# Optimization experiments

Hardware: AMD Instinct MI355X
Metric: run time of the kernel (lower is better)

Reference implementation:

```python
import jax, jax.numpy as jnp
import numpy as np

N_S, N_C, N_L = 100000, 20000, 5000
E_U, E_T = 2000000, 500000
D_S, D_C, D_L, H = 64, 32, 128, 128
N_LAYERS = 3  # num_layers=2 -> ModuleList holds 3 hetero layers


def _sage(h_src, h_dst, src_idx, dst_idx, W_self, W_neigh, b, n_dst):
    # DGL SAGEConv 'mean': fc_self(h_dst) + fc_neigh(mean of in-neighbor src feats) + bias
    summed = jax.ops.segment_sum(h_src[src_idx], dst_idx, num_segments=n_dst)  # [n_dst, d]
    deg = jax.ops.segment_sum(jnp.ones((src_idx.shape[0],), h_src.dtype), dst_idx, num_segments=n_dst)
    h_neigh = summed / jnp.maximum(deg, 1.0)[:, None]
    return h_dst @ W_self + h_neigh @ W_neigh + b


def setup_inputs() -> dict:
    key = jax.random.key(0)
    ks = jax.random.split(key, 24)
    s = 0.05
    inp = {
        'feat_student': jax.random.normal(ks[0], (N_S, D_S), jnp.float32),
        'feat_concept': jax.random.normal(ks[1], (N_C, D_C), jnp.float32),
        'feat_lecture': jax.random.normal(ks[2], (N_L, D_L), jnp.float32),
        'W_fs': jax.random.normal(ks[3], (D_S, H), jnp.float32) * s,
        'b_fs': jnp.zeros((H,), jnp.float32),
        'W_fc': jax.random.normal(ks[4], (D_C, H), jnp.float32) * s,
        'b_fc': jnp.zeros((H,), jnp.float32),
        'W_fl': jax.random.normal(ks[5], (D_L, H), jnp.float32) * s,
        'b_fl': jnp.zeros((H,), jnp.float32),
        # per-layer, per-relation SAGE params (all dims 128 so they stack)
        'W_self_u': jax.random.normal(ks[6], (N_LAYERS, H, H), jnp.float32) * s,
        'W_neigh_u': jax.random.normal(ks[7], (N_LAYERS, H, H), jnp.float32) * s,
        'b_u': jnp.zeros((N_LAYERS, H), jnp.float32),
        'W_self_t': jax.random.normal(ks[8], (N_LAYERS, H, H), jnp.float32) * s,
        'W_neigh_t': jax.random.normal(ks[9], (N_LAYERS, H, H), jnp.float32) * s,
        'b_t': jnp.zeros((N_LAYERS, H), jnp.float32),
        'und_src': jax.random.randint(ks[10], (E_U,), 0, N_S, jnp.int32),
        'und_dst': jax.random.randint(ks[11], (E_U,), 0, N_C, jnp.int32),
        'tea_src': jax.random.randint(ks[12], (E_T,), 0, N_L, jnp.int32),
        'tea_dst': jax.random.randint(ks[13], (E_T,), 0, N_C, jnp.int32),
    }
    return inp


def reference(feat_student, feat_concept, feat_lecture,
              W_fs, b_fs, W_fc, b_fc, W_fl, b_fl,
              W_self_u, W_neigh_u, b_u, W_self_t, W_neigh_t, b_t,
              und_src, und_dst, tea_src, tea_dst):
    # input projections per node type
    h_s = feat_student @ W_fs + b_fs
    h_c = feat_concept @ W_fc + b_fc
    h_l = feat_lecture @ W_fl + b_fl
    n_c = h_c.shape[0]
    for i in range(N_LAYERS):
        ou = _sage(h_s, h_c, und_src, und_dst, W_self_u[i], W_neigh_u[i], b_u[i], n_c)
        ot = _sage(h_l, h_c, tea_src, tea_dst, W_self_t[i], W_neigh_t[i], b_t[i], n_c)
        # HeteroGraphConv cross-relation aggregate: 'mean' on layer 0, default 'sum' after
        h_c = (ou + ot) * (0.5 if i == 0 else 1.0)
        if i != N_LAYERS - 1:
            h_c = jax.nn.relu(h_c)  # dropout is identity in eval mode
        # student/lecture are never destination types -> features pass through
    return h_c  # [N_C, 128] concept embeddings
```

## Files before the change

kernel.cpp:

```cpp
#include <hip/hip_runtime.h>
#include <hip/hip_bf16.h>
#include <cstdint>
#include <cstddef>

#define NS_ 100000
#define NC_ 20000
#define NL_ 5000
#define EU_ 2000000
#define ET_ 500000
#define H_  128

#define NBK_ 625
#define CHK_ 3907
#define UBLK_ 512
#define TBLK_ 128
#define CAPU_ 3600
#define CAPT_ 1024
#define SEDGE_ 3712
#define SROW_ 640

typedef __attribute__((ext_vector_type(8))) short bs8;
typedef __attribute__((ext_vector_type(4))) float f32x4;
typedef __attribute__((ext_vector_type(2))) float v2f;

__device__ inline short bf_rne(float f) {
    unsigned u = __float_as_uint(f);
    u = (u + 0x7fffu + ((u >> 16) & 1u)) >> 16;
    return (short)u;
}
__device__ inline unsigned pack_bf16x2(float a, float b) {
    return ((unsigned)(unsigned short)bf_rne(a)) |
           (((unsigned)(unsigned short)bf_rne(b)) << 16);
}
__device__ inline float bflo(unsigned w) { return __uint_as_float(w << 16); }
__device__ inline float bfhi(unsigned w) { return __uint_as_float(w & 0xffff0000u); }

#define B_SCU UBLK_
#define B_SCT TBLK_
#define B_CVT 512
#define B_PACK 480
#define B_BC 2
#define B_WFC 16
#define B_TOTAL (B_SCU + B_SCT + B_CVT + B_PACK + B_BC + B_WFC)

__global__ __launch_bounds__(256) void prep_fused_kernel(
    const int* __restrict__ und_dst, const int* __restrict__ tea_dst,
    unsigned* __restrict__ CUm, unsigned* __restrict__ CTm,
    const float* __restrict__ feat_s, unsigned* __restrict__ fs8,
    const float* __restrict__ feat_l, unsigned* __restrict__ flb,
    const float* __restrict__ Wsu, const float* __restrict__ Wnu,
    const float* __restrict__ Wst, const float* __restrict__ Wnt,
    const float* __restrict__ W_fs, const float* __restrict__ W_fl,
    short* __restrict__ WpL,
    const float* __restrict__ bu, const float* __restrict__ bt,
    const float* __restrict__ b_fs, const float* __restrict__ b_fl,
    float* __restrict__ bc,
    const float* __restrict__ W_fc, short* __restrict__ WpC)
{
    __shared__ unsigned cnt[768];
    const int b = blockIdx.x;
    const int tid = threadIdx.x;

    if (b < B_SCU + B_SCT) {
        const bool isU = (b < B_SCU);
        const int blk = isU ? b : (b - B_SCU);
        const int nEdge = isU ? EU_ : ET_;
        const int* dstp = isU ? und_dst : tea_dst;
        unsigned* Cm = isU ? CUm : CTm;
        for (int i = tid; i < 768; i += 256) cnt[i] = 0;
        __syncthreads();
        const int start = blk * CHK_;
        const int end = min(start + CHK_, nEdge);
        for (int i = start + tid; i < end; i += 256)
            atomicAdd(&cnt[dstp[i] >> 5], 1u);
        __syncthreads();
        for (int i = tid; i < NBK_; i += 256)
            Cm[(size_t)blk * SROW_ + i] = cnt[i];
    } else if (b < B_SCU + B_SCT + B_CVT) {
        int i = (b - B_SCU - B_SCT) * 256 + tid;
        const int stride = B_CVT * 256;
        const int nS = NS_ * 16;
        const int nTot = nS + NL_ * 64;
        for (; i < nTot; i += stride) {
            if (i < nS) {
                const float4 v = ((const float4*)feat_s)[i];
                unsigned r = __builtin_amdgcn_cvt_pk_fp8_f32(v.x, v.y, 0, false);
                r = __builtin_amdgcn_cvt_pk_fp8_f32(v.z, v.w, r, true);
                fs8[i] = r;
            } else {
                int j = i - nS;
                float2 v = ((const float2*)feat_l)[j];
                flb[j] = pack_bf16x2(v.x, v.y);
            }
        }
    } else if (b < B_SCU + B_SCT + B_CVT + B_PACK) {
        int i = (b - B_SCU - B_SCT - B_CVT) * 256 + tid;
        int j = i & 7;
        int lane = (i >> 3) & 63;
        int nt = (i >> 9) & 7;
        int ktAll = i >> 12;
        int l = ktAll / 10;
        int kt = ktAll - l * 10;
        int k = kt * 32 + (lane >> 4) * 8 + j;
        int n = nt * 16 + (lane & 15);
        const size_t WL = (size_t)l * H_ * H_;
        float v;
        if (k < 128) {
            v = Wsu[WL + k * H_ + n] + Wst[WL + k * H_ + n];
        } else if (k < 192) {
            int a = k - 128;
            v = 0.f;
            for (int t = 0; t < 128; t++) v += W_fs[a * H_ + t] * Wnu[WL + t * H_ + n];
        } else {
            int a = k - 192;
            v = 0.f;
            for (int t = 0; t < 128; t++) v += W_fl[a * H_ + t] * Wnt[WL + t * H_ + n];
        }
        WpL[i] = bf_rne(v);
    } else if (b < B_SCU + B_SCT + B_CVT + B_PACK + B_BC) {
        int i = (b - B_SCU - B_SCT - B_CVT - B_PACK) * 256 + tid;
        if (i < 3 * H_) {
            int l = i >> 7, c = i & 127;
            const size_t WL = (size_t)l * H_ * H_;
            float v = bu[i] + bt[i];
            for (int j2 = 0; j2 < 128; j2++)
                v += b_fs[j2] * Wnu[WL + j2 * H_ + c] + b_fl[j2] * Wnt[WL + j2 * H_ + c];
            bc[i] = v;
        }
    } else {
        int i = (b - (B_SCU + B_SCT + B_CVT + B_PACK + B_BC)) * 256 + tid;
        int j = i & 7;
        int lane = (i >> 3) & 63;
        int nt = (i >> 9) & 7;
        int k = (lane >> 4) * 8 + j;
        int n = nt * 16 + (lane & 15);
        WpC[i] = bf_rne(W_fc[k * H_ + n]);
    }
}

__global__ __launch_bounds__(256) void scan_kernel(
    const unsigned* __restrict__ CUm, const unsigned* __restrict__ CTm,
    unsigned* __restrict__ OUm, unsigned* __restrict__ OTm,
    unsigned* __restrict__ gcurU, unsigned* __restrict__ gcurT)
{
    __shared__ unsigned part[4][64];
    const int b = blockIdx.x;
    const int tid = threadIdx.x;
    const int s = tid >> 6;
    const int kl = tid & 63;
    const int k = b * 64 + kl;
    const bool ok = (k < NBK_);

    {
        unsigned run = 0;
        const int r0 = s * 128;
        if (ok) {
#pragma unroll 8
            for (int r = r0; r < r0 + 128; ++r)
                run += CUm[(size_t)r * SROW_ + k];
        }
        part[s][kl] = run;
        __syncthreads();
        unsigned base = 0;
        for (int s2 = 0; s2 < s; ++s2) base += part[s2][kl];
        if (ok && s == 3) gcurU[k] = base + run;
        if (ok) {
            unsigned acc = base;
#pragma unroll 8
            for (int r = r0; r < r0 + 128; ++r) {
                unsigned c = CUm[(size_t)r * SROW_ + k];
                OUm[(size_t)r * SROW_ + k] = acc;
                acc += c;
            }
        }
        __syncthreads();
    }
    {
        unsigned run = 0;
        const int r0 = s * 32;
        if (ok) {
#pragma unroll 8
            for (int r = r0; r < r0 + 32; ++r)
                run += CTm[(size_t)r * SROW_ + k];
        }
        part[s][kl] = run;
        __syncthreads();
        unsigned base = 0;
        for (int s2 = 0; s2 < s; ++s2) base += part[s2][kl];
        if (ok && s == 3) gcurT[k] = base + run;
        if (ok) {
            unsigned acc = base;
#pragma unroll 8
            for (int r = r0; r < r0 + 32; ++r) {
                unsigned c = CTm[(size_t)r * SROW_ + k];
                OTm[(size_t)r * SROW_ + k] = acc;
                acc += c;
            }
        }
    }
}

__global__ __launch_bounds__(256) void scatter_kernel(
    const int* __restrict__ und_dst, const int* __restrict__ und_src,
    const int* __restrict__ tea_dst, const int* __restrict__ tea_src,
    const unsigned* __restrict__ CUm, const unsigned* __restrict__ CTm,
    const unsigned* __restrict__ OUm, const unsigned* __restrict__ OTm,
    unsigned* __restrict__ binnedU, unsigned* __restrict__ binnedT)
{
    __shared__ unsigned smem[5760];
    const int b = blockIdx.x;
    const int tid = threadIdx.x;
    const bool isU = (b < B_SCU);
    const int blk = isU ? b : (b - B_SCU);
    const int nEdge = isU ? EU_ : ET_;
    const int* dstp = isU ? und_dst : tea_dst;
    const int* srcp = isU ? und_src : tea_src;
    const unsigned* Cm = isU ? CUm : CTm;
    const unsigned* Om = isU ? OUm : OTm;
    unsigned* binned = isU ? binnedU : binnedT;
    const unsigned cap = isU ? CAPU_ : CAPT_;
    unsigned* sed = smem;
    unsigned* cnt = smem + 3968;
    unsigned* pre = smem + 4736;
    unsigned* par = smem + 5504;

    unsigned Wr[3];
#pragma unroll
    for (int r = 0; r < 3; r++) {
        int k = r * 256 + tid;
        cnt[k] = (k < NBK_) ? Cm[(size_t)blk * SROW_ + k] : 0;
        Wr[r] = (k < NBK_) ? Om[(size_t)blk * SROW_ + k] : 0;
    }
    __syncthreads();
    unsigned c0 = cnt[3 * tid], c1 = cnt[3 * tid + 1], c2 = cnt[3 * tid + 2];
    unsigned s = c0 + c1 + c2;
    par[tid] = s;
    __syncthreads();
    unsigned sum = s;
    for (int d = 1; d < 256; d <<= 1) {
        unsigned x = (tid >= d) ? par[tid - d] : 0;
        __syncthreads();
        sum += x;
        par[tid] = sum;
        __syncthreads();
    }
    unsigned p = sum - s;
    pre[3 * tid] = p;
    pre[3 * tid + 1] = p + c0;
    pre[3 * tid + 2] = p + c0 + c1;
    __syncthreads();
#pragma unroll
    for (int r = 0; r < 3; r++) {
        int k = r * 256 + tid;
        if (k < NBK_) {
            unsigned L = cnt[k];
            unsigned W = Wr[r];
            if (W + L > cap) W = (L <= cap) ? cap - L : 0;
            cnt[k] = k * cap + W - pre[k];
        }
    }
    __syncthreads();
    const int start = blk * CHK_;
    const int end = min(start + CHK_, nEdge);
    for (int i = start + tid; i < end; i += 256) {
        int d = dstp[i];
        unsigned k = (unsigned)d >> 5;
        unsigned e = (unsigned)srcp[i] | ((unsigned)(d & 31) << 17) | (k << 22);
        unsigned pos = atomicAdd(&pre[k], 1u);
        sed[pos] = e;
    }
    __syncthreads();
    const int n = end - start;
    for (int i = tid; i < n; i += 256) {
        unsigned e = sed[i];
        binned[cnt[e >> 22] + i] = e & 0x3FFFFFu;
    }
}

__global__ __launch_bounds__(256) void agg_kernel(
    const unsigned* __restrict__ gcurU, const unsigned* __restrict__ binnedU,
    const uint2* __restrict__ fs8, unsigned* __restrict__ aggFu,
    const unsigned* __restrict__ gcurT, const unsigned* __restrict__ binnedT,
    const uint4* __restrict__ flb4, unsigned* __restrict__ aggFt)
{
    __shared__ unsigned sedge[SEDGE_];
    __shared__ unsigned sh[32], soff[33], scur[32];
    const int b = blockIdx.x;
    const int tid = threadIdx.x;
    const bool isU = (b < NBK_);
    const int bb = isU ? b : (b - NBK_);
    const unsigned* binned = isU ? binnedU : binnedT;
    const unsigned cap = isU ? CAPU_ : CAPT_;
    const size_t start = (size_t)bb * cap;
    const int n = min((int)(isU ? gcurU : gcurT)[bb], (int)cap);

    if (tid < 32) sh[tid] = 0;
    __syncthreads();
    for (int i = tid; i < n; i += 256)
        atomicAdd(&sh[(binned[start + i] >> 17) & 31], 1u);
    __syncthreads();
    if (tid == 0) {
        unsigned r = 0;
        for (int j = 0; j < 32; j++) {
            unsigned v = sh[j];
            soff[j] = r;
            scur[j] = r;
            r += v;
        }
        soff[32] = r;
    }
    __syncthreads();
    for (int i = tid; i < n; i += 256) {
        unsigned p = binned[start + i];
        unsigned pos = atomicAdd(&scur[(p >> 17) & 31], 1u);
        if (pos < SEDGE_) sedge[pos] = p & 0x1FFFFu;
    }
    __syncthreads();

    const int g = tid >> 3;
    const int sub = tid & 7;
    const int gs = (int)soff[g];
    const int ge = (int)min(soff[g + 1], (unsigned)SEDGE_);
    const int c = bb * 32 + g;
    const float inv = 1.f / (float)max(ge - gs, 1);

    if (isU) {
        float a[8];
#pragma unroll
        for (int i = 0; i < 8; i++) a[i] = 0.f;
        int e = gs;
        for (; e + 4 <= ge; e += 4) {
            unsigned s0 = sedge[e], s1 = sedge[e + 1];
            unsigned s2 = sedge[e + 2], s3 = sedge[e + 3];
            uint2 w0 = fs8[(size_t)s0 * 8 + sub];
            uint2 w1 = fs8[(size_t)s1 * 8 + sub];
            uint2 w2 = fs8[(size_t)s2 * 8 + sub];
            uint2 w3 = fs8[(size_t)s3 * 8 + sub];
            v2f p0, p1, p2, p3;
            p0 = __builtin_amdgcn_cvt_pk_f32_fp8(w0.x, false);
            p1 = __builtin_amdgcn_cvt_pk_f32_fp8(w0.x, true);
            p2 = __builtin_amdgcn_cvt_pk_f32_fp8(w0.y, false);
            p3 = __builtin_amdgcn_cvt_pk_f32_fp8(w0.y, true);
            a[0] += p0.x; a[1] += p0.y; a[2] += p1.x; a[3] += p1.y;
            a[4] += p2.x; a[5] += p2.y; a[6] += p3.x; a[7] += p3.y;
            p0 = __builtin_amdgcn_cvt_pk_f32_fp8(w1.x, false);
            p1 = __builtin_amdgcn_cvt_pk_f32_fp8(w1.x, true);
            p2 = __builtin_amdgcn_cvt_pk_f32_fp8(w1.y, false);
            p3 = __builtin_amdgcn_cvt_pk_f32_fp8(w1.y, true);
            a[0] += p0.x; a[1] += p0.y; a[2] += p1.x; a[3] += p1.y;
            a[4] += p2.x; a[5] += p2.y; a[6] += p3.x; a[7] += p3.y;
            p0 = __builtin_amdgcn_cvt_pk_f32_fp8(w2.x, false);
            p1 = __builtin_amdgcn_cvt_pk_f32_fp8(w2.x, true);
            p2 = __builtin_amdgcn_cvt_pk_f32_fp8(w2.y, false);
            p3 = __builtin_amdgcn_cvt_pk_f32_fp8(w2.y, true);
            a[0] += p0.x; a[1] += p0.y; a[2] += p1.x; a[3] += p1.y;
            a[4] += p2.x; a[5] += p2.y; a[6] += p3.x; a[7] += p3.y;
            p0 = __builtin_amdgcn_cvt_pk_f32_fp8(w3.x, false);
            p1 = __builtin_amdgcn_cvt_pk_f32_fp8(w3.x, true);
            p2 = __builtin_amdgcn_cvt_pk_f32_fp8(w3.y, false);
            p3 = __builtin_amdgcn_cvt_pk_f32_fp8(w3.y, true);
            a[0] += p0.x; a[1] += p0.y; a[2] += p1.x; a[3] += p1.y;
            a[4] += p2.x; a[5] += p2.y; a[6] += p3.x; a[7] += p3.y;
        }
        for (; e < ge; e++) {
            uint2 w0 = fs8[(size_t)sedge[e] * 8 + sub];
            v2f p0 = __builtin_amdgcn_cvt_pk_f32_fp8(w0.x, false);
            v2f p1 = __builtin_amdgcn_cvt_pk_f32_fp8(w0.x, true);
            v2f p2 = __builtin_amdgcn_cvt_pk_f32_fp8(w0.y, false);
            v2f p3 = __builtin_amdgcn_cvt_pk_f32_fp8(w0.y, true);
            a[0] += p0.x; a[1] += p0.y; a[2] += p1.x; a[3] += p1.y;
            a[4] += p2.x; a[5] += p2.y; a[6] += p3.x; a[7] += p3.y;
        }
        uint4 o;
        o.x = pack_bf16x2(a[0] * inv, a[1] * inv);
        o.y = pack_bf16x2(a[2] * inv, a[3] * inv);
        o.z = pack_bf16x2(a[4] * inv, a[5] * inv);
        o.w = pack_bf16x2(a[6] * inv, a[7] * inv);
        ((uint4*)aggFu)[(size_t)c * 8 + sub] = o;
    } else {
        float a[16];
#pragma unroll
        for (int i = 0; i < 16; i++) a[i] = 0.f;
        int e = gs;
        for (; e + 2 <= ge; e += 2) {
            unsigned s0 = sedge[e], s1 = sedge[e + 1];
            uint4 w0 = flb4[(size_t)s0 * 16 + sub * 2];
            uint4 w1 = flb4[(size_t)s0 * 16 + sub * 2 + 1];
            uint4 x0 = flb4[(size_t)s1 * 16 + sub * 2];
            uint4 x1 = flb4[(size_t)s1 * 16 + sub * 2 + 1];
            a[0] += bflo(w0.x); a[1] += bfhi(w0.x);
            a[2] += bflo(w0.y); a[3] += bfhi(w0.y);
            a[4] += bflo(w0.z); a[5] += bfhi(w0.z);
            a[6] += bflo(w0.w); a[7] += bfhi(w0.w);
            a[8]  += bflo(w1.x); a[9]  += bfhi(w1.x);
            a[10] += bflo(w1.y); a[11] += bfhi(w1.y);
            a[12] += bflo(w1.z); a[13] += bfhi(w1.z);
            a[14] += bflo(w1.w); a[15] += bfhi(w1.w);
            a[0] += bflo(x0.x); a[1] += bfhi(x0.x);
            a[2] += bflo(x0.y); a[3] += bfhi(x0.y);
            a[4] += bflo(x0.z); a[5] += bfhi(x0.z);
            a[6] += bflo(x0.w); a[7] += bfhi(x0.w);
            a[8]  += bflo(x1.x); a[9]  += bfhi(x1.x);
            a[10] += bflo(x1.y); a[11] += bfhi(x1.y);
            a[12] += bflo(x1.z); a[13] += bfhi(x1.z);
            a[14] += bflo(x1.w); a[15] += bfhi(x1.w);
        }
        if (e < ge) {
            unsigned src = sedge[e];
            uint4 w0 = flb4[(size_t)src * 16 + sub * 2];
            uint4 w1 = flb4[(size_t)src * 16 + sub * 2 + 1];
            a[0] += bflo(w0.x); a[1] += bfhi(w0.x);
            a[2] += bflo(w0.y); a[3] += bfhi(w0.y);
            a[4] += bflo(w0.z); a[5] += bfhi(w0.z);
            a[6] += bflo(w0.w); a[7] += bfhi(w0.w);
            a[8]  += bflo(w1.x); a[9]  += bfhi(w1.x);
            a[10] += bflo(w1.y); a[11] += bfhi(w1.y);
            a[12] += bflo(w1.z); a[13] += bfhi(w1.z);
            a[14] += bflo(w1.w); a[15] += bfhi(w1.w);
        }
        uint4 o0, o1;
        o0.x = pack_bf16x2(a[0] * inv, a[1] * inv);
        o0.y = pack_bf16x2(a[2] * inv, a[3] * inv);
        o0.z = pack_bf16x2(a[4] * inv, a[5] * inv);
        o0.w = pack_bf16x2(a[6] * inv, a[7] * inv);
        o1.x = pack_bf16x2(a[8] * inv, a[9] * inv);
        o1.y = pack_bf16x2(a[10] * inv, a[11] * inv);
        o1.z = pack_bf16x2(a[12] * inv, a[13] * inv);
        o1.w = pack_bf16x2(a[14] * inv, a[15] * inv);
        ((uint4*)aggFt)[(size_t)c * 16 + sub * 2] = o0;
        ((uint4*)aggFt)[(size_t)c * 16 + sub * 2 + 1] = o1;
    }
}

__global__ __launch_bounds__(256) void layers_fused_kernel(
    const float* __restrict__ feat_c, const short* __restrict__ WpC,
    const float* __restrict__ b_fc,
    const unsigned* __restrict__ aggFu, const unsigned* __restrict__ aggFt,
    const short* __restrict__ WpL, const float* __restrict__ bc,
    float* __restrict__ out)
{
    __shared__ short lds[2][16 * 132];
    const int tid = threadIdx.x;
    const int lane = tid & 63;
    const int wv = tid >> 6;
    const int gr = wv >> 1;
    const int h = wv & 1;
    const int row0 = blockIdx.x * 32 + gr * 16;
    const int q = lane >> 4;
    const int m = lane & 15;
    const int rA = min(row0 + m, NC_ - 1);
    short* tile = lds[gr];

    bs8 fuF[2], ftF[4], hcF[4];
#pragma unroll
    for (int kt = 0; kt < 2; kt++)
        fuF[kt] = *(const bs8*)(aggFu + (size_t)rA * 32 + kt * 16 + q * 4);
#pragma unroll
    for (int kt = 0; kt < 4; kt++)
        ftF[kt] = *(const bs8*)(aggFt + (size_t)rA * 64 + kt * 16 + q * 4);

    f32x4 acc[4];
#pragma unroll
    for (int i = 0; i < 4; i++) acc[i] = (f32x4){0.f, 0.f, 0.f, 0.f};
    {
        const float* xp = feat_c + (size_t)rA * 32 + q * 8;
        float4 xa = *(const float4*)xp;
        float4 xb = *(const float4*)(xp + 4);
        bs8 af;
        af[0] = bf_rne(xa.x); af[1] = bf_rne(xa.y); af[2] = bf_rne(xa.z); af[3] = bf_rne(xa.w);
        af[4] = bf_rne(xb.x); af[5] = bf_rne(xb.y); af[6] = bf_rne(xb.z); af[7] = bf_rne(xb.w);
#pragma unroll
        for (int nt = 0; nt < 4; nt++) {
            int ntg = h * 4 + nt;
            bs8 bfr = *(const bs8*)(WpC + ((size_t)ntg * 64 + lane) * 8);
            acc[nt] = __builtin_amdgcn_mfma_f32_16x16x32_bf16(af, bfr, acc[nt], 0, 0, 0);
        }
    }
#pragma unroll
    for (int nt = 0; nt < 4; nt++) {
        int col = (h * 4 + nt) * 16 + m;
        float bv = b_fc[col];
#pragma unroll
        for (int r = 0; r < 4; r++)
            tile[(q * 4 + r) * 132 + col] = bf_rne(acc[nt][r] + bv);
    }
    __syncthreads();
#pragma unroll
    for (int kt = 0; kt < 4; kt++)
        hcF[kt] = *(const bs8*)(tile + m * 132 + kt * 32 + q * 8);
    __syncthreads();

#pragma unroll
    for (int l = 0; l < 3; l++) {
#pragma unroll
        for (int i = 0; i < 4; i++) acc[i] = (f32x4){0.f, 0.f, 0.f, 0.f};
        const short* wl = WpL + (size_t)l * 40960;
#pragma unroll
        for (int kt = 0; kt < 10; kt++) {
            bs8 af = (kt < 4) ? hcF[kt] : ((kt < 6) ? fuF[kt - 4] : ftF[kt - 6]);
            const short* wp = wl + (size_t)kt * 4096;
#pragma unroll
            for (int nt = 0; nt < 4; nt++) {
                int ntg = h * 4 + nt;
                bs8 bfr = *(const bs8*)(wp + ((size_t)ntg * 64 + lane) * 8);
                acc[nt] = __builtin_amdgcn_mfma_f32_16x16x32_bf16(af, bfr, acc[nt], 0, 0, 0);
            }
        }
        const float scale = (l == 0) ? 0.5f : 1.0f;
        const float* bl = bc + l * H_;
        if (l < 2) {
#pragma unroll
            for (int nt = 0; nt < 4; nt++) {
                int col = (h * 4 + nt) * 16 + m;
                float bv = bl[col];
#pragma unroll
                for (int r = 0; r < 4; r++)
                    tile[(q * 4 + r) * 132 + col] =
                        bf_rne(fmaxf((acc[nt][r] + bv) * scale, 0.f));
            }
            __syncthreads();
#pragma unroll
            for (int kt = 0; kt < 4; kt++)
                hcF[kt] = *(const bs8*)(tile + m * 132 + kt * 32 + q * 8);
            __syncthreads();
        } else {
#pragma unroll
            for (int nt = 0; nt < 4; nt++) {
                int col = (h * 4 + nt) * 16 + m;
                float bv = bl[col];
#pragma unroll
                for (int r = 0; r < 4; r++) {
                    int row = row0 + q * 4 + r;
                    if (row < NC_)
                        out[(size_t)row * H_ + col] = (acc[nt][r] + bv) * scale;
                }
            }
        }
    }
}

extern "C" void kernel_launch(void* const* d_in, const int* in_sizes, int n_in,
                              void* d_out, int out_size, void* d_ws, size_t ws_size,
                              hipStream_t stream)
{
    (void)in_sizes; (void)n_in; (void)out_size; (void)ws_size;
    const float* feat_s = (const float*)d_in[0];
    const float* feat_c = (const float*)d_in[1];
    const float* feat_l = (const float*)d_in[2];
    const float* W_fs = (const float*)d_in[3];
    const float* b_fs = (const float*)d_in[4];
    const float* W_fc = (const float*)d_in[5];
    const float* b_fc = (const float*)d_in[6];
    const float* W_fl = (const float*)d_in[7];
    const float* b_fl = (const float*)d_in[8];
    const float* W_self_u  = (const float*)d_in[9];
    const float* W_neigh_u = (const float*)d_in[10];
    const float* b_u = (const float*)d_in[11];
    const float* W_self_t  = (const float*)d_in[12];
    const float* W_neigh_t = (const float*)d_in[13];
    const float* b_t = (const float*)d_in[14];
    const int* und_src = (const int*)d_in[15];
    const int* und_dst = (const int*)d_in[16];
    const int* tea_src = (const int*)d_in[17];
    const int* tea_dst = (const int*)d_in[18];
    float* out = (float*)d_out;

    char* ws = (char*)d_ws;
    size_t o = 0;
    auto alloc = [&](size_t bytes) -> char* {
        char* p = ws + o;
        o += (bytes + 255) & ~(size_t)255;
        return p;
    };
    unsigned* fs8  = (unsigned*)alloc((size_t)NS_ * 16 * 4);
    unsigned* flb  = (unsigned*)alloc((size_t)NL_ * 64 * 4);
    unsigned* aggFu = (unsigned*)alloc((size_t)NC_ * 32 * 4);
    unsigned* aggFt = (unsigned*)alloc((size_t)NC_ * 64 * 4);
    short* WpL = (short*)alloc((size_t)3 * 10 * 8 * 64 * 8 * 2);
    short* WpC = (short*)alloc((size_t)8 * 64 * 8 * 2);
    float* bc  = (float*)alloc((size_t)3 * H_ * 4);
    unsigned* gcurU = (unsigned*)alloc((size_t)NBK_ * 4);
    unsigned* gcurT = (unsigned*)alloc((size_t)NBK_ * 4);
    unsigned* binnedU = (unsigned*)alloc((size_t)NBK_ * CAPU_ * 4);
    unsigned* binnedT = (unsigned*)alloc((size_t)NBK_ * CAPT_ * 4);

    unsigned* CUm = aggFt;
    unsigned* OUm = aggFt + (size_t)UBLK_ * SROW_;
    unsigned* CTm = aggFt + (size_t)2 * UBLK_ * SROW_;
    unsigned* OTm = CTm + (size_t)TBLK_ * SROW_;

    prep_fused_kernel<<<B_TOTAL, 256, 0, stream>>>(
        und_dst, tea_dst, CUm, CTm,
        feat_s, fs8, feat_l, flb,
        W_self_u, W_neigh_u, W_self_t, W_neigh_t, W_fs, W_fl, WpL,
        b_u, b_t, b_fs, b_fl, bc,
        W_fc, WpC);

    scan_kernel<<<10, 256, 0, stream>>>(CUm, CTm, OUm, OTm, gcurU, gcurT);

    scatter_kernel<<<B_SCU + B_SCT, 256, 0, stream>>>(
        und_dst, und_src, tea_dst, tea_src,
        CUm, CTm, OUm, OTm, binnedU, binnedT);

    agg_kernel<<<2 * NBK_, 256, 0, stream>>>(
        gcurU, binnedU, (const uint2*)fs8, aggFu,
        gcurT, binnedT, (const uint4*)flb, aggFt);

    layers_fused_kernel<<<(NC_ + 31) / 32, 256, 0, stream>>>(
        feat_c, WpC, b_fc, aggFu, aggFt, WpL, bc, out);
}
```

Before: 207.1 us.

## Raise parallelism across scatter, aggregation and layer kernels

Halves the edge chunk size so twice as many scatter blocks run, with the scan kernel reworked to cover the larger count matrices. Each concept's edge list in the aggregation kernel is now split between two 8-lane groups inside 512-thread blocks, and the partial sums are combined with a shuffle. The fused layer kernel now gives each block 16 rows instead of 32, with each wave computing two output column tiles. The aim is more occupancy and latency hiding on gather-heavy stages, at the cost of more blocks, duplicated weight loads per row tile, and separate workspace for the count matrices instead of aliasing aggFt.

```diff
diff --git a/kernel.cpp b/kernel.cpp
--- a/kernel.cpp
+++ b/kernel.cpp
@@ -11,9 +11,9 @@
 #define H_  128
 
 #define NBK_ 625
-#define CHK_ 3907
-#define UBLK_ 512
-#define TBLK_ 128
+#define CHK_ 1954
+#define UBLK_ 1024
+#define TBLK_ 256
 #define CAPU_ 3600
 #define CAPT_ 1024
 #define SEDGE_ 3712
@@ -143,12 +143,12 @@
     unsigned* __restrict__ OUm, unsigned* __restrict__ OTm,
     unsigned* __restrict__ gcurU, unsigned* __restrict__ gcurT)
 {
-    __shared__ unsigned part[4][64];
+    __shared__ unsigned part[8][32];
     const int b = blockIdx.x;
     const int tid = threadIdx.x;
-    const int s = tid >> 6;
-    const int kl = tid & 63;
-    const int k = b * 64 + kl;
+    const int s = tid >> 5;
+    const int kl = tid & 31;
+    const int k = b * 32 + kl;
     const bool ok = (k < NBK_);
 
     {
@@ -163,7 +163,7 @@
         __syncthreads();
         unsigned base = 0;
         for (int s2 = 0; s2 < s; ++s2) base += part[s2][kl];
-        if (ok && s == 3) gcurU[k] = base + run;
+        if (ok && s == 7) gcurU[k] = base + run;
         if (ok) {
             unsigned acc = base;
 #pragma unroll 8
@@ -187,7 +187,7 @@
         __syncthreads();
         unsigned base = 0;
         for (int s2 = 0; s2 < s; ++s2) base += part[s2][kl];
-        if (ok && s == 3) gcurT[k] = base + run;
+        if (ok && s == 7) gcurT[k] = base + run;
         if (ok) {
             unsigned acc = base;
 #pragma unroll 8
@@ -207,7 +207,7 @@
     const unsigned* __restrict__ OUm, const unsigned* __restrict__ OTm,
     unsigned* __restrict__ binnedU, unsigned* __restrict__ binnedT)
 {
-    __shared__ unsigned smem[5760];
+    __shared__ unsigned smem[3776];
     const int b = blockIdx.x;
     const int tid = threadIdx.x;
     const bool isU = (b < B_SCU);
@@ -220,9 +220,9 @@
     unsigned* binned = isU ? binnedU : binnedT;
     const unsigned cap = isU ? CAPU_ : CAPT_;
     unsigned* sed = smem;
-    unsigned* cnt = smem + 3968;
-    unsigned* pre = smem + 4736;
-    unsigned* par = smem + 5504;
+    unsigned* cnt = smem + 1984;
+    unsigned* pre = smem + 2752;
+    unsigned* par = smem + 3520;
 
     unsigned Wr[3];
 #pragma unroll
@@ -277,7 +277,7 @@
     }
 }
 
-__global__ __launch_bounds__(256) void agg_kernel(
+__global__ __launch_bounds__(512) void agg_kernel(
     const unsigned* __restrict__ gcurU, const unsigned* __restrict__ binnedU,
     const uint2* __restrict__ fs8, unsigned* __restrict__ aggFu,
     const unsigned* __restrict__ gcurT, const unsigned* __restrict__ binnedT,
@@ -296,7 +296,7 @@
 
     if (tid < 32) sh[tid] = 0;
     __syncthreads();
-    for (int i = tid; i < n; i += 256)
+    for (int i = tid; i < n; i += 512)
         atomicAdd(&sh[(binned[start + i] >> 17) & 31], 1u);
     __syncthreads();
     if (tid == 0) {
@@ -310,26 +310,31 @@
         soff[32] = r;
     }
     __syncthreads();
-    for (int i = tid; i < n; i += 256) {
+    for (int i = tid; i < n; i += 512) {
         unsigned p = binned[start + i];
         unsigned pos = atomicAdd(&scur[(p >> 17) & 31], 1u);
         if (pos < SEDGE_) sedge[pos] = p & 0x1FFFFu;
     }
     __syncthreads();
 
-    const int g = tid >> 3;
+    const int g = tid >> 4;
+    const int half = (tid >> 3) & 1;
     const int sub = tid & 7;
     const int gs = (int)soff[g];
     const int ge = (int)min(soff[g + 1], (unsigned)SEDGE_);
+    const int len = ge - gs;
+    const int mid = gs + ((len + 1) >> 1);
+    const int es = half ? mid : gs;
+    const int ee = half ? ge : mid;
     const int c = bb * 32 + g;
-    const float inv = 1.f / (float)max(ge - gs, 1);
+    const float inv = 1.f / (float)max(len, 1);
 
     if (isU) {
         float a[8];
 #pragma unroll
         for (int i = 0; i < 8; i++) a[i] = 0.f;
-        int e = gs;
-        for (; e + 4 <= ge; e += 4) {
+        int e = es;
+        for (; e + 4 <= ee; e += 4) {
             unsigned s0 = sedge[e], s1 = sedge[e + 1];
             unsigned s2 = sedge[e + 2], s3 = sedge[e + 3];
             uint2 w0 = fs8[(size_t)s0 * 8 + sub];
@@ -362,7 +367,7 @@
             a[0] += p0.x; a[1] += p0.y; a[2] += p1.x; a[3] += p1.y;
             a[4] += p2.x; a[5] += p2.y; a[6] += p3.x; a[7] += p3.y;
         }
-        for (; e < ge; e++) {
+        for (; e < ee; e++) {
             uint2 w0 = fs8[(size_t)sedge[e] * 8 + sub];
             v2f p0 = __builtin_amdgcn_cvt_pk_f32_fp8(w0.x, false);
             v2f p1 = __builtin_amdgcn_cvt_pk_f32_fp8(w0.x, true);
@@ -371,18 +376,22 @@
             a[0] += p0.x; a[1] += p0.y; a[2] += p1.x; a[3] += p1.y;
             a[4] += p2.x; a[5] += p2.y; a[6] += p3.x; a[7] += p3.y;
         }
-        uint4 o;
-        o.x = pack_bf16x2(a[0] * inv, a[1] * inv);
-        o.y = pack_bf16x2(a[2] * inv, a[3] * inv);
-        o.z = pack_bf16x2(a[4] * inv, a[5] * inv);
-        o.w = pack_bf16x2(a[6] * inv, a[7] * inv);
-        ((uint4*)aggFu)[(size_t)c * 8 + sub] = o;
+#pragma unroll
+        for (int i = 0; i < 8; i++) a[i] += __shfl_xor(a[i], 8);
+        if (half == 0) {
+            uint4 o;
+            o.x = pack_bf16x2(a[0] * inv, a[1] * inv);
+            o.y = pack_bf16x2(a[2] * inv, a[3] * inv);
+            o.z = pack_bf16x2(a[4] * inv, a[5] * inv);
+            o.w = pack_bf16x2(a[6] * inv, a[7] * inv);
+            ((uint4*)aggFu)[(size_t)c * 8 + sub] = o;
+        }
     } else {
         float a[16];
 #pragma unroll
         for (int i = 0; i < 16; i++) a[i] = 0.f;
-        int e = gs;
-        for (; e + 2 <= ge; e += 2) {
+        int e = es;
+        for (; e + 2 <= ee; e += 2) {
             unsigned s0 = sedge[e], s1 = sedge[e + 1];
             uint4 w0 = flb4[(size_t)s0 * 16 + sub * 2];
             uint4 w1 = flb4[(size_t)s0 * 16 + sub * 2 + 1];
@@ -405,7 +414,7 @@
             a[12] += bflo(x1.z); a[13] += bfhi(x1.z);
             a[14] += bflo(x1.w); a[15] += bfhi(x1.w);
         }
-        if (e < ge) {
+        if (e < ee) {
             unsigned src = sedge[e];
             uint4 w0 = flb4[(size_t)src * 16 + sub * 2];
             uint4 w1 = flb4[(size_t)src * 16 + sub * 2 + 1];
@@ -418,17 +427,21 @@
             a[12] += bflo(w1.z); a[13] += bfhi(w1.z);
             a[14] += bflo(w1.w); a[15] += bfhi(w1.w);
         }
-        uint4 o0, o1;
-        o0.x = pack_bf16x2(a[0] * inv, a[1] * inv);
-        o0.y = pack_bf16x2(a[2] * inv, a[3] * inv);
-        o0.z = pack_bf16x2(a[4] * inv, a[5] * inv);
-        o0.w = pack_bf16x2(a[6] * inv, a[7] * inv);
-        o1.x = pack_bf16x2(a[8] * inv, a[9] * inv);
-        o1.y = pack_bf16x2(a[10] * inv, a[11] * inv);
-        o1.z = pack_bf16x2(a[12] * inv, a[13] * inv);
-        o1.w = pack_bf16x2(a[14] * inv, a[15] * inv);
-        ((uint4*)aggFt)[(size_t)c * 16 + sub * 2] = o0;
-        ((uint4*)aggFt)[(size_t)c * 16 + sub * 2 + 1] = o1;
+#pragma unroll
+        for (int i = 0; i < 16; i++) a[i] += __shfl_xor(a[i], 8);
+        if (half == 0) {
+            uint4 o0, o1;
+            o0.x = pack_bf16x2(a[0] * inv, a[1] * inv);
+            o0.y = pack_bf16x2(a[2] * inv, a[3] * inv);
+            o0.z = pack_bf16x2(a[4] * inv, a[5] * inv);
+            o0.w = pack_bf16x2(a[6] * inv, a[7] * inv);
+            o1.x = pack_bf16x2(a[8] * inv, a[9] * inv);
+            o1.y = pack_bf16x2(a[10] * inv, a[11] * inv);
+            o1.z = pack_bf16x2(a[12] * inv, a[13] * inv);
+            o1.w = pack_bf16x2(a[14] * inv, a[15] * inv);
+            ((uint4*)aggFt)[(size_t)c * 16 + sub * 2] = o0;
+            ((uint4*)aggFt)[(size_t)c * 16 + sub * 2 + 1] = o1;
+        }
     }
 }
 
@@ -439,17 +452,14 @@
     const short* __restrict__ WpL, const float* __restrict__ bc,
     float* __restrict__ out)
 {
-    __shared__ short lds[2][16 * 132];
+    __shared__ short tile[16 * 132];
     const int tid = threadIdx.x;
     const int lane = tid & 63;
     const int wv = tid >> 6;
-    const int gr = wv >> 1;
-    const int h = wv & 1;
-    const int row0 = blockIdx.x * 32 + gr * 16;
+    const int row0 = blockIdx.x * 16;
     const int q = lane >> 4;
     const int m = lane & 15;
     const int rA = min(row0 + m, NC_ - 1);
-    short* tile = lds[gr];
 
     bs8 fuF[2], ftF[4], hcF[4];
 #pragma unroll
@@ -459,9 +469,9 @@
     for (int kt = 0; kt < 4; kt++)
         ftF[kt] = *(const bs8*)(aggFt + (size_t)rA * 64 + kt * 16 + q * 4);
 
-    f32x4 acc[4];
-#pragma unroll
-    for (int i = 0; i < 4; i++) acc[i] = (f32x4){0.f, 0.f, 0.f, 0.f};
+    f32x4 acc[2];
+#pragma unroll
+    for (int i = 0; i < 2; i++) acc[i] = (f32x4){0.f, 0.f, 0.f, 0.f};
     {
         const float* xp = feat_c + (size_t)rA * 32 + q * 8;
         float4 xa = *(const float4*)xp;
@@ -470,15 +480,15 @@
         af[0] = bf_rne(xa.x); af[1] = bf_rne(xa.y); af[2] = bf_rne(xa.z); af[3] = bf_rne(xa.w);
         af[4] = bf_rne(xb.x); af[5] = bf_rne(xb.y); af[6] = bf_rne(xb.z); af[7] = bf_rne(xb.w);
 #pragma unroll
-        for (int nt = 0; nt < 4; nt++) {
-            int ntg = h * 4 + nt;
+        for (int nt = 0; nt < 2; nt++) {
+            int ntg = wv * 2 + nt;
             bs8 bfr = *(const bs8*)(WpC + ((size_t)ntg * 64 + lane) * 8);
             acc[nt] = __builtin_amdgcn_mfma_f32_16x16x32_bf16(af, bfr, acc[nt], 0, 0, 0);
         }
     }
 #pragma unroll
-    for (int nt = 0; nt < 4; nt++) {
-        int col = (h * 4 + nt) * 16 + m;
+    for (int nt = 0; nt < 2; nt++) {
+        int col = (wv * 2 + nt) * 16 + m;
         float bv = b_fc[col];
 #pragma unroll
         for (int r = 0; r < 4; r++)
@@ -493,15 +503,15 @@
 #pragma unroll
     for (int l = 0; l < 3; l++) {
 #pragma unroll
-        for (int i = 0; i < 4; i++) acc[i] = (f32x4){0.f, 0.f, 0.f, 0.f};
+        for (int i = 0; i < 2; i++) acc[i] = (f32x4){0.f, 0.f, 0.f, 0.f};
         const short* wl = WpL + (size_t)l * 40960;
 #pragma unroll
         for (int kt = 0; kt < 10; kt++) {
             bs8 af = (kt < 4) ? hcF[kt] : ((kt < 6) ? fuF[kt - 4] : ftF[kt - 6]);
             const short* wp = wl + (size_t)kt * 4096;
 #pragma unroll
-            for (int nt = 0; nt < 4; nt++) {
-                int ntg = h * 4 + nt;
+            for (int nt = 0; nt < 2; nt++) {
+                int ntg = wv * 2 + nt;
                 bs8 bfr = *(const bs8*)(wp + ((size_t)ntg * 64 + lane) * 8);
                 acc[nt] = __builtin_amdgcn_mfma_f32_16x16x32_bf16(af, bfr, acc[nt], 0, 0, 0);
             }
@@ -510,8 +520,8 @@
         const float* bl = bc + l * H_;
         if (l < 2) {
 #pragma unroll
-            for (int nt = 0; nt < 4; nt++) {
-                int col = (h * 4 + nt) * 16 + m;
+            for (int nt = 0; nt < 2; nt++) {
+                int col = (wv * 2 + nt) * 16 + m;
                 float bv = bl[col];
 #pragma unroll
                 for (int r = 0; r < 4; r++)
@@ -525,8 +535,8 @@
             __syncthreads();
         } else {
 #pragma unroll
-            for (int nt = 0; nt < 4; nt++) {
-                int col = (h * 4 + nt) * 16 + m;
+            for (int nt = 0; nt < 2; nt++) {
+                int col = (wv * 2 + nt) * 16 + m;
                 float bv = bl[col];
 #pragma unroll
                 for (int r = 0; r < 4; r++) {
@@ -583,11 +593,10 @@
     unsigned* gcurT = (unsigned*)alloc((size_t)NBK_ * 4);
     unsigned* binnedU = (unsigned*)alloc((size_t)NBK_ * CAPU_ * 4);
     unsigned* binnedT = (unsigned*)alloc((size_t)NBK_ * CAPT_ * 4);
-
-    unsigned* CUm = aggFt;
-    unsigned* OUm = aggFt + (size_t)UBLK_ * SROW_;
-    unsigned* CTm = aggFt + (size_t)2 * UBLK_ * SROW_;
-    unsigned* OTm = CTm + (size_t)TBLK_ * SROW_;
+    unsigned* CUm = (unsigned*)alloc((size_t)UBLK_ * SROW_ * 4);
+    unsigned* OUm = (unsigned*)alloc((size_t)UBLK_ * SROW_ * 4);
+    unsigned* CTm = (unsigned*)alloc((size_t)TBLK_ * SROW_ * 4);
+    unsigned* OTm = (unsigned*)alloc((size_t)TBLK_ * SROW_ * 4);
 
     prep_fused_kernel<<<B_TOTAL, 256, 0, stream>>>(
         und_dst, tea_dst, CUm, CTm,
@@ -596,16 +605,16 @@
         b_u, b_t, b_fs, b_fl, bc,
         W_fc, WpC);
 
-    scan_kernel<<<10, 256, 0, stream>>>(CUm, CTm, OUm, OTm, gcurU, gcurT);
+    scan_kernel<<<20, 256, 0, stream>>>(CUm, CTm, OUm, OTm, gcurU, gcurT);
 
     scatter_kernel<<<B_SCU + B_SCT, 256, 0, stream>>>(
         und_dst, und_src, tea_dst, tea_src,
         CUm, CTm, OUm, OTm, binnedU, binnedT);
 
-    agg_kernel<<<2 * NBK_, 256, 0, stream>>>(
+    agg_kernel<<<2 * NBK_, 512, 0, stream>>>(
         gcurU, binnedU, (const uint2*)fs8, aggFu,
         gcurT, binnedT, (const uint4*)flb, aggFt);
 
-    layers_fused_kernel<<<(NC_ + 31) / 32, 256, 0, stream>>>(
+    layers_fused_kernel<<<(NC_ + 15) / 16, 256, 0, stream>>>(
         feat_c, WpC, b_fc, aggFu, aggFt, WpL, bc, out);
 }
```

Result: no change. 205.8 us (-0.6%).
